# Optimization experiments

Hardware: AMD Instinct MI355X
Metric: run time of the kernel (lower is better)

## Reference

```python
import jax, jax.numpy as jnp
import numpy as np

B, S, D, H = 4, 2048, 1024, 16
DH = D // H


def setup_inputs() -> dict:
    key = jax.random.key(0)
    ks = jax.random.split(key, 11)
    s = 1.0 / np.sqrt(D)
    return {
        "q": jax.random.normal(ks[0], (B, S, D), jnp.float32),
        "k": jax.random.normal(ks[1], (B, S, D), jnp.float32),
        "v": jax.random.normal(ks[2], (B, S, D), jnp.float32),
        "Wq": jax.random.normal(ks[3], (D, D), jnp.float32) * s,
        "bq": jnp.zeros((D,), jnp.float32),
        "Wk": jax.random.normal(ks[4], (D, D), jnp.float32) * s,
        "bk": jnp.zeros((D,), jnp.float32),
        "Wv": jax.random.normal(ks[5], (D, D), jnp.float32) * s,
        "bv": jnp.zeros((D,), jnp.float32),
        "Wo": jax.random.normal(ks[6], (D, D), jnp.float32) * s,
        "bo": jnp.zeros((D,), jnp.float32),
    }


def _split_heads(x):
    # (B, S, D) -> (B, H, S, DH)
    b, s, _ = x.shape
    return x.reshape(b, s, H, DH).transpose(0, 2, 1, 3)


def reference(q, k, v, Wq, bq, Wk, bk, Wv, bv, Wo, bo):
    # torch Linear: x @ W.T + b
    qh = _split_heads(q @ Wq.T + bq)
    kh = _split_heads(k @ Wk.T + bk)
    vh = _split_heads(v @ Wv.T + bv)
    scale = 1.0 / jnp.sqrt(jnp.asarray(DH, qh.dtype))
    scores = jnp.einsum("bhqd,bhkd->bhqk", qh, kh) * scale  # (B,H,S,S)
    probs = jax.nn.softmax(scores, axis=-1)
    ctx = jnp.einsum("bhqk,bhkd->bhqd", probs, vh)  # (B,H,S,DH)
    x = ctx.transpose(0, 2, 1, 3).reshape(q.shape[0], -1, D)
    return x @ Wo.T + bo
```

## Files before the change

kernel.cpp:

```cpp
#include <hip/hip_runtime.h>

typedef __bf16 bf16x8 __attribute__((ext_vector_type(8)));
typedef __bf16 bf16x4 __attribute__((ext_vector_type(4)));
typedef _Float16 f16x4v __attribute__((ext_vector_type(4)));
typedef float f32x4 __attribute__((ext_vector_type(4)));
typedef float f32x16 __attribute__((ext_vector_type(16)));
typedef unsigned short u16;
typedef unsigned int u32;

constexpr int Bc = 4, Sc = 2048, Dc = 1024, Hc = 16, DHc = 64;
constexpr int Mrows = Bc * Sc;
constexpr size_t MK = (size_t)Mrows * Dc;
constexpr size_t WK = (size_t)Dc * Dc;

__device__ __forceinline__ u16 f2bf(float f) {
  u32 u = __float_as_uint(f);
  u = (u + 0x7fffu + ((u >> 16) & 1u)) >> 16;
  return (u16)u;
}

#define LDSP(p) ((__attribute__((address_space(3))) void*)(p))
#define GLBP(p) ((const __attribute__((address_space(1))) void*)(p))

__global__ __launch_bounds__(256) void cvt3_kernel(const float* __restrict__ a,
                                                   const float* __restrict__ b,
                                                   const float* __restrict__ c,
                                                   ushort4* __restrict__ out, int n4) {
  const float4* in = (const float4*)(blockIdx.y == 0 ? a : blockIdx.y == 1 ? b : c);
  ushort4* o = out + (size_t)blockIdx.y * n4;
  int stride = gridDim.x * blockDim.x;
  for (int i = blockIdx.x * blockDim.x + threadIdx.x; i < n4; i += stride) {
    float4 v = in[i];
    ushort4 r;
    r.x = f2bf(v.x); r.y = f2bf(v.y); r.z = f2bf(v.z); r.w = f2bf(v.w);
    o[i] = r;
  }
}

__global__ __launch_bounds__(256) void cvt4_kernel(const float* __restrict__ a,
                                                   const float* __restrict__ b,
                                                   const float* __restrict__ c,
                                                   const float* __restrict__ d,
                                                   ushort4* __restrict__ out, int n4) {
  const float4* in = (const float4*)(blockIdx.y == 0 ? a : blockIdx.y == 1 ? b
                                     : blockIdx.y == 2 ? c : d);
  ushort4* o = out + (size_t)blockIdx.y * n4;
  int stride = gridDim.x * blockDim.x;
  for (int i = blockIdx.x * blockDim.x + threadIdx.x; i < n4; i += stride) {
    float4 v = in[i];
    ushort4 r;
    r.x = f2bf(v.x); r.y = f2bf(v.y); r.z = f2bf(v.z); r.w = f2bf(v.w);
    o[i] = r;
  }
}

enum GemmMode { MODE_Q = 0, MODE_K = 1, MODE_V = 2, MODE_OUT = 3 };

template <int FUSED3>
__global__ __launch_bounds__(512, 2) void gemm8(const u16* __restrict__ A0,
                                                const u16* __restrict__ Bt0,
                                                const float* __restrict__ b0,
                                                const float* __restrict__ b1,
                                                const float* __restrict__ b2,
                                                void* __restrict__ out0) {
  constexpr int K = 1024, NT = 16;
  __shared__ u16 lds[3 * 24576];

  const int y = FUSED3 ? (int)blockIdx.y : 3;
  const u16* A = A0 + (FUSED3 ? (size_t)blockIdx.y * MK : 0);
  const u16* Bt = Bt0 + (FUSED3 ? (size_t)blockIdx.y * WK : 0);
  const float* bias = FUSED3 ? (y == 0 ? b0 : y == 1 ? b1 : b2) : b0;

  const int wg = (blockIdx.x & 7) * 32 + (blockIdx.x >> 3);
  const int tm = wg >> 3, tn = wg & 7;
  const int row0 = tm << 8, col0 = tn << 7;

  const int t_ = threadIdx.x, w = t_ >> 6, l = t_ & 63;
  const int wm = w >> 1, wn = w & 1;
  const int col = l & 31, hh = l >> 5;

  f32x16 acc[2][2] = {};

  auto stA = [&](int tile, int i) {
    u16* buf = &lds[(tile % 3) * 24576];
    const int c = (w * 4 + i) * 64 + l;
    const int r = c >> 3, gl = c & 7;
    __builtin_amdgcn_global_load_lds(
        GLBP(A + (size_t)(row0 + r) * K + (tile << 6) + ((gl ^ (r & 7)) << 3)),
        LDSP(buf + (w * 4 + i) * 512), 16, 0, 0);
  };
  auto stB = [&](int tile, int i) {
    u16* buf = &lds[(tile % 3) * 24576] + 16384;
    const int c = (w * 2 + i) * 64 + l;
    const int r = c >> 3, gl = c & 7;
    __builtin_amdgcn_global_load_lds(
        GLBP(Bt + (size_t)(col0 + r) * K + (tile << 6) + ((gl ^ (r & 7)) << 3)),
        LDSP(buf + (w * 2 + i) * 512), 16, 0, 0);
  };

#pragma unroll
  for (int i = 0; i < 4; ++i) stA(0, i);
#pragma unroll
  for (int i = 0; i < 2; ++i) stB(0, i);
#pragma unroll
  for (int i = 0; i < 4; ++i) stA(1, i);
#pragma unroll
  for (int i = 0; i < 2; ++i) stB(1, i);
  asm volatile("s_waitcnt vmcnt(6)" ::: "memory");
  __builtin_amdgcn_s_barrier();

  const int ar0 = wm * 64 + col, ar1 = ar0 + 32;
  const int br0 = wn * 64 + col, br1 = br0 + 32;

#pragma unroll 1
  for (int t = 0; t < NT; ++t) {
    const u16* abuf = &lds[(t % 3) * 24576];
    const u16* bbuf = abuf + 16384;
#pragma unroll
    for (int ph = 0; ph < 2; ++ph) {
      bf16x8 a0[2], a1[2], q0[2], q1[2];
#pragma unroll
      for (int k2 = 0; k2 < 2; ++k2) {
        const int ks = ph * 2 + k2;
        a0[k2] = *(const bf16x8*)&abuf[ar0 * 64 + ((((ks << 1) + hh) ^ (ar0 & 7)) << 3)];
        a1[k2] = *(const bf16x8*)&abuf[ar1 * 64 + ((((ks << 1) + hh) ^ (ar1 & 7)) << 3)];
        q0[k2] = *(const bf16x8*)&bbuf[br0 * 64 + ((((ks << 1) + hh) ^ (br0 & 7)) << 3)];
        q1[k2] = *(const bf16x8*)&bbuf[br1 * 64 + ((((ks << 1) + hh) ^ (br1 & 7)) << 3)];
      }
      if (t + 2 < NT) {
        if (ph == 0) { stA(t + 2, 0); stA(t + 2, 1); stA(t + 2, 2); }
        else         { stA(t + 2, 3); stB(t + 2, 0); stB(t + 2, 1); }
      }
      __builtin_amdgcn_sched_barrier(0);
      __builtin_amdgcn_s_barrier();
      __builtin_amdgcn_sched_barrier(0);
      __builtin_amdgcn_s_setprio(1);
#pragma unroll
      for (int k2 = 0; k2 < 2; ++k2) {
        acc[0][0] = __builtin_amdgcn_mfma_f32_32x32x16_bf16(a0[k2], q0[k2], acc[0][0], 0, 0, 0);
        acc[0][1] = __builtin_amdgcn_mfma_f32_32x32x16_bf16(a0[k2], q1[k2], acc[0][1], 0, 0, 0);
        acc[1][0] = __builtin_amdgcn_mfma_f32_32x32x16_bf16(a1[k2], q0[k2], acc[1][0], 0, 0, 0);
        acc[1][1] = __builtin_amdgcn_mfma_f32_32x32x16_bf16(a1[k2], q1[k2], acc[1][1], 0, 0, 0);
      }
      __builtin_amdgcn_s_setprio(0);
      __builtin_amdgcn_sched_barrier(0);
    }
    if (t + 2 < NT)      asm volatile("s_waitcnt vmcnt(6)" ::: "memory");
    else if (t + 1 < NT) asm volatile("s_waitcnt vmcnt(0)" ::: "memory");
    __builtin_amdgcn_s_barrier();
  }

#pragma unroll
  for (int mi = 0; mi < 2; ++mi)
#pragma unroll
    for (int ni = 0; ni < 2; ++ni) {
      const int n = col0 + wn * 64 + ni * 32 + col;
      const float bv = bias[n];
      const int mbase = row0 + wm * 64 + mi * 32 + 4 * hh;
      if (y == 3) {
        float* O = (float*)out0;
#pragma unroll
        for (int r = 0; r < 16; ++r) {
          const int m = mbase + (r & 3) + 8 * (r >> 2);
          O[(size_t)m * Dc + n] = acc[mi][ni][r] + bv;
        }
      } else if (y == 2) {
        u16* Vt = (u16*)out0 + 2 * MK;
        const int h = n >> 6, dh = n & 63;
#pragma unroll
        for (int qg = 0; qg < 4; ++qg) {
          const int s0 = mbase + 8 * qg;
          const int b = s0 >> 11, s = s0 & (Sc - 1);
          f16x4v pk;
#pragma unroll
          for (int r4 = 0; r4 < 4; ++r4) pk[r4] = (_Float16)(acc[mi][ni][qg * 4 + r4] + bv);
          *(f16x4v*)&Vt[((size_t)((b * Hc + h) * DHc + dh)) * Sc + s] = pk;
        }
      } else {
        u16* Oh = (u16*)out0 + (size_t)y * MK;
        const float scl = (y == 0) ? 0.125f * 1.44269504089f : 1.f;
        const int h = n >> 6, dh = n & 63;
#pragma unroll
        for (int r = 0; r < 16; ++r) {
          const int m = mbase + (r & 3) + 8 * (r >> 2);
          const int b = m >> 11, s = m & (Sc - 1);
          Oh[((size_t)((b * Hc + h) * Sc + s)) * DHc + dh] = f2bf((acc[mi][ni][r] + bv) * scl);
        }
      }
    }
}

__global__ __launch_bounds__(256, 2) void attn3_kernel(const u16* __restrict__ Qh,
                                                       const u16* __restrict__ Kh,
                                                       const u16* __restrict__ Vt,
                                                       u16* __restrict__ ctx) {
  __shared__ u16 smem[16384];
  u16* K_lds = smem;
  u16* V_lds = smem + 8192;

  const int wid = (blockIdx.x & 7) * 128 + (blockIdx.x >> 3);
  const int qt = wid & 15, bh = wid >> 4;
  const int t = threadIdx.x, w = t >> 6, l = t & 63;
  const int q = l & 31, h = l >> 5;
  const int q0 = qt * 128 + w * 32;

  bf16x8 qf[4];
  {
    const u16* qp = Qh + ((size_t)bh * Sc + q0 + q) * DHc + h * 8;
#pragma unroll
    for (int kk = 0; kk < 4; ++kk) qf[kk] = *(const bf16x8*)(qp + kk * 16);
  }

  f32x16 oacc[2] = {};
  float m_run = -3.0e38f, l_run = 0.f;

  for (int kt = 0; kt < Sc; kt += 128) {
    __syncthreads();
#pragma unroll
    for (int c = 0; c < 4; ++c) {
      const int kb = (w * 4 + c) * 8;
      const int row = kb + (l >> 3);
      const int sg = (l & 7) ^ (row & 7);
      __builtin_amdgcn_global_load_lds(GLBP(Kh + ((size_t)bh * Sc + kt + row) * DHc + sg * 8),
                                       LDSP(&K_lds[kb * 64]), 16, 0, 0);
    }
#pragma unroll
    for (int c = 0; c < 4; ++c) {
      const int vb = (w * 4 + c) * 4;
      const int row = vb + (l >> 4);
      const int sg = (l & 15) ^ (row & 15);
      __builtin_amdgcn_global_load_lds(GLBP(Vt + ((size_t)bh * DHc + row) * Sc + kt + sg * 8),
                                       LDSP(&V_lds[vb * 128]), 16, 0, 0);
    }
    __syncthreads();

#pragma unroll
    for (int h64 = 0; h64 < 2; ++h64) {
      f32x16 sacc[2];
#pragma unroll
      for (int kt32 = 0; kt32 < 2; ++kt32) {
        f32x16 s_ = {};
        const int krow = h64 * 64 + kt32 * 32 + q;
        __builtin_amdgcn_s_setprio(1);
#pragma unroll
        for (int kk = 0; kk < 4; ++kk) {
          bf16x8 kf = *(const bf16x8*)&K_lds[krow * 64 + ((2 * kk + h) ^ (krow & 7)) * 8];
          s_ = __builtin_amdgcn_mfma_f32_32x32x16_bf16(kf, qf[kk], s_, 0, 0, 0);
        }
        __builtin_amdgcn_s_setprio(0);
        sacc[kt32] = s_;
      }

      float mx = sacc[0][0];
#pragma unroll
      for (int r = 1; r < 16; ++r) mx = fmaxf(mx, sacc[0][r]);
#pragma unroll
      for (int r = 0; r < 16; ++r) mx = fmaxf(mx, sacc[1][r]);
      mx = fmaxf(mx, __shfl_xor(mx, 32));
      if (__any(mx - m_run > 8.f)) {
        const float mnew = fmaxf(m_run, mx);
        const float corr = __builtin_amdgcn_exp2f(m_run - mnew);
        m_run = mnew;
        l_run *= corr;
#pragma unroll
        for (int dt = 0; dt < 2; ++dt)
#pragma unroll
          for (int r = 0; r < 16; ++r) oacc[dt][r] *= corr;
      }
      float sum = 0.f;
      f16x4v pa[2][4];
#pragma unroll
      for (int kt32 = 0; kt32 < 2; ++kt32)
#pragma unroll
        for (int kc = 0; kc < 4; ++kc)
#pragma unroll
          for (int j = 0; j < 4; ++j) {
            float pv = __builtin_amdgcn_exp2f(sacc[kt32][kc * 4 + j] - m_run);
            sum += pv;
            pa[kt32][kc][j] = (_Float16)pv;
          }
      sum += __shfl_xor(sum, 32);
      l_run += sum;

      __builtin_amdgcn_s_setprio(1);
#pragma unroll
      for (int kt32 = 0; kt32 < 2; ++kt32)
#pragma unroll
        for (int kc = 0; kc < 4; ++kc)
#pragma unroll
          for (int dt = 0; dt < 2; ++dt) {
            const int vrow = dt * 32 + q;
            const int kslot = h64 * 8 + kt32 * 4 + kc;
            f16x4v vf = *(const f16x4v*)&V_lds[vrow * 128 + ((kslot ^ (vrow & 15)) * 8) + 4 * h];
            oacc[dt] = __builtin_amdgcn_mfma_f32_32x32x8f16(vf, pa[kt32][kc], oacc[dt], 0, 0, 0);
          }
      __builtin_amdgcn_s_setprio(0);
    }
  }

  __syncthreads();
  const float inv = 1.f / l_run;
  u16* E = smem + w * 2048;
#pragma unroll
  for (int dt = 0; dt < 2; ++dt)
#pragma unroll
    for (int rg = 0; rg < 4; ++rg) {
      bf16x4 pk;
#pragma unroll
      for (int j = 0; j < 4; ++j) pk[j] = (__bf16)(oacc[dt][rg * 4 + j] * inv);
      const int dh0 = dt * 32 + rg * 8 + 4 * h;
      int byte = q * 128 + dh0 * 2;
      byte ^= (q & 7) << 4;
      *(bf16x4*)((char*)E + byte) = pk;
    }
  __syncthreads();
  const int b = bh >> 4, head = bh & 15;
  const size_t crow = ((size_t)(b * Sc + q0 + q)) * Dc + head * 64 + h * 32;
#pragma unroll
  for (int i = 0; i < 4; ++i) {
    const int g = (4 * h + i) ^ (q & 7);
    uint4 tv = *(const uint4*)((char*)E + q * 128 + g * 16);
    *(uint4*)((u16*)ctx + crow + i * 8) = tv;
  }
}

extern "C" void kernel_launch(void* const* d_in, const int* in_sizes, int n_in,
                              void* d_out, int out_size, void* d_ws, size_t ws_size,
                              hipStream_t stream) {
  const float* q  = (const float*)d_in[0];
  const float* k  = (const float*)d_in[1];
  const float* v  = (const float*)d_in[2];
  const float* Wq = (const float*)d_in[3];
  const float* bq = (const float*)d_in[4];
  const float* Wk = (const float*)d_in[5];
  const float* bk = (const float*)d_in[6];
  const float* Wv = (const float*)d_in[7];
  const float* bv = (const float*)d_in[8];
  const float* Wo = (const float*)d_in[9];
  const float* bo = (const float*)d_in[10];
  float* out = (float*)d_out;

  u16* qb  = (u16*)d_ws;
  u16* Wqb = qb + 3 * MK;
  u16* Qh  = Wqb + 4 * WK;
  u16* Kh  = Qh + MK;
  u16* VtB = Kh + MK;
  u16* ctx = VtB + MK;

  cvt3_kernel<<<dim3(2048, 3), 256, 0, stream>>>(q, k, v, (ushort4*)qb, (int)(MK / 4));
  cvt4_kernel<<<dim3(512, 4), 256, 0, stream>>>(Wq, Wk, Wv, Wo, (ushort4*)Wqb, (int)(WK / 4));

  gemm8<1><<<dim3(256, 3), 512, 0, stream>>>(qb, Wqb, bq, bk, bv, (void*)Qh);

  attn3_kernel<<<1024, 256, 0, stream>>>(Qh, Kh, VtB, ctx);

  gemm8<0><<<dim3(256, 1), 512, 0, stream>>>(ctx, Wqb + 3 * WK, bo, bo, bo, (void*)out);
}
```

Before: 236.6 us.

## Double-buffer attention K/V tiles and use permlane-swapped 32x32x16 f16 MFMA for PV

Measured after the change: 220.5 us. 1.07x faster.

```diff
diff --git a/kernel.cpp b/kernel.cpp
--- a/kernel.cpp
+++ b/kernel.cpp
@@ -2,11 +2,13 @@
 
 typedef __bf16 bf16x8 __attribute__((ext_vector_type(8)));
 typedef __bf16 bf16x4 __attribute__((ext_vector_type(4)));
+typedef _Float16 f16x8 __attribute__((ext_vector_type(8)));
 typedef _Float16 f16x4v __attribute__((ext_vector_type(4)));
 typedef float f32x4 __attribute__((ext_vector_type(4)));
 typedef float f32x16 __attribute__((ext_vector_type(16)));
 typedef unsigned short u16;
 typedef unsigned int u32;
+typedef unsigned int u32x4 __attribute__((ext_vector_type(4)));
 
 constexpr int Bc = 4, Sc = 2048, Dc = 1024, Hc = 16, DHc = 64;
 constexpr int Mrows = Bc * Sc;
@@ -53,8 +55,6 @@
     o[i] = r;
   }
 }
-
-enum GemmMode { MODE_Q = 0, MODE_K = 1, MODE_V = 2, MODE_OUT = 3 };
 
 template <int FUSED3>
 __global__ __launch_bounds__(512, 2) void gemm8(const u16* __restrict__ A0,
@@ -190,7 +190,7 @@
     }
 }
 
-__global__ __launch_bounds__(256, 2) void attn3_kernel(const u16* __restrict__ Qh,
+__global__ __launch_bounds__(256, 4) void attn4_kernel(const u16* __restrict__ Qh,
                                                        const u16* __restrict__ Kh,
                                                        const u16* __restrict__ Vt,
                                                        u16* __restrict__ ctx) {
@@ -214,91 +214,101 @@
   f32x16 oacc[2] = {};
   float m_run = -3.0e38f, l_run = 0.f;
 
-  for (int kt = 0; kt < Sc; kt += 128) {
-    __syncthreads();
-#pragma unroll
-    for (int c = 0; c < 4; ++c) {
-      const int kb = (w * 4 + c) * 8;
-      const int row = kb + (l >> 3);
-      const int sg = (l & 7) ^ (row & 7);
+  const int lrow = l >> 3, lg = l & 7;
+
+  auto stage = [&](int tile, int buf) {
+    const int kt = tile << 6;
+    u16* Kb = K_lds + buf * 4096;
+    u16* Vb = V_lds + buf * 4096;
+#pragma unroll
+    for (int c = 0; c < 2; ++c) {
+      const int rb = w * 16 + c * 8;
+      const int row = rb + lrow;
+      const int sg = lg ^ (row & 7);
       __builtin_amdgcn_global_load_lds(GLBP(Kh + ((size_t)bh * Sc + kt + row) * DHc + sg * 8),
-                                       LDSP(&K_lds[kb * 64]), 16, 0, 0);
-    }
-#pragma unroll
-    for (int c = 0; c < 4; ++c) {
-      const int vb = (w * 4 + c) * 4;
-      const int row = vb + (l >> 4);
-      const int sg = (l & 15) ^ (row & 15);
+                                       LDSP(&Kb[rb * 64]), 16, 0, 0);
       __builtin_amdgcn_global_load_lds(GLBP(Vt + ((size_t)bh * DHc + row) * Sc + kt + sg * 8),
-                                       LDSP(&V_lds[vb * 128]), 16, 0, 0);
-    }
-    __syncthreads();
-
-#pragma unroll
-    for (int h64 = 0; h64 < 2; ++h64) {
-      f32x16 sacc[2];
-#pragma unroll
-      for (int kt32 = 0; kt32 < 2; ++kt32) {
-        f32x16 s_ = {};
-        const int krow = h64 * 64 + kt32 * 32 + q;
+                                       LDSP(&Vb[rb * 64]), 16, 0, 0);
+    }
+  };
+
+  stage(0, 0);
+  __syncthreads();
+
+#pragma unroll 1
+  for (int tile = 0; tile < 32; ++tile) {
+    const int cur = tile & 1;
+    if (tile + 1 < 32) stage(tile + 1, cur ^ 1);
+    const u16* Kb = K_lds + cur * 4096;
+    const u16* Vb = V_lds + cur * 4096;
+
+    f32x16 sacc[2] = {};
+    __builtin_amdgcn_s_setprio(1);
+#pragma unroll
+    for (int kk = 0; kk < 4; ++kk) {
+      const int kr0 = q, kr1 = 32 + q;
+      bf16x8 kf0 = *(const bf16x8*)&Kb[kr0 * 64 + ((2 * kk + h) ^ (kr0 & 7)) * 8];
+      bf16x8 kf1 = *(const bf16x8*)&Kb[kr1 * 64 + ((2 * kk + h) ^ (kr1 & 7)) * 8];
+      sacc[0] = __builtin_amdgcn_mfma_f32_32x32x16_bf16(kf0, qf[kk], sacc[0], 0, 0, 0);
+      sacc[1] = __builtin_amdgcn_mfma_f32_32x32x16_bf16(kf1, qf[kk], sacc[1], 0, 0, 0);
+    }
+    __builtin_amdgcn_s_setprio(0);
+
+    float mx = sacc[0][0];
+#pragma unroll
+    for (int r = 1; r < 16; ++r) mx = fmaxf(mx, sacc[0][r]);
+#pragma unroll
+    for (int r = 0; r < 16; ++r) mx = fmaxf(mx, sacc[1][r]);
+    mx = fmaxf(mx, __shfl_xor(mx, 32));
+    if (__any(mx - m_run > 8.f)) {
+      const float mnew = fmaxf(m_run, mx);
+      const float corr = __builtin_amdgcn_exp2f(m_run - mnew);
+      m_run = mnew;
+      l_run *= corr;
+#pragma unroll
+      for (int dt = 0; dt < 2; ++dt)
+#pragma unroll
+        for (int r = 0; r < 16; ++r) oacc[dt][r] *= corr;
+    }
+
+    float sum = 0.f;
+#pragma unroll
+    for (int kt32 = 0; kt32 < 2; ++kt32)
+#pragma unroll
+      for (int c = 0; c < 2; ++c) {
+        float p0 = __builtin_amdgcn_exp2f(sacc[kt32][c * 8 + 0] - m_run);
+        float p1 = __builtin_amdgcn_exp2f(sacc[kt32][c * 8 + 1] - m_run);
+        float p2 = __builtin_amdgcn_exp2f(sacc[kt32][c * 8 + 2] - m_run);
+        float p3 = __builtin_amdgcn_exp2f(sacc[kt32][c * 8 + 3] - m_run);
+        float p4 = __builtin_amdgcn_exp2f(sacc[kt32][c * 8 + 4] - m_run);
+        float p5 = __builtin_amdgcn_exp2f(sacc[kt32][c * 8 + 5] - m_run);
+        float p6 = __builtin_amdgcn_exp2f(sacc[kt32][c * 8 + 6] - m_run);
+        float p7 = __builtin_amdgcn_exp2f(sacc[kt32][c * 8 + 7] - m_run);
+        sum += ((p0 + p1) + (p2 + p3)) + ((p4 + p5) + (p6 + p7));
+        u32 X0 = __builtin_bit_cast(u32, __builtin_amdgcn_cvt_pkrtz(p0, p1));
+        u32 X1 = __builtin_bit_cast(u32, __builtin_amdgcn_cvt_pkrtz(p2, p3));
+        u32 Y0 = __builtin_bit_cast(u32, __builtin_amdgcn_cvt_pkrtz(p4, p5));
+        u32 Y1 = __builtin_bit_cast(u32, __builtin_amdgcn_cvt_pkrtz(p6, p7));
+        auto rA = __builtin_amdgcn_permlane32_swap(X0, Y0, false, false);
+        auto rB = __builtin_amdgcn_permlane32_swap(X1, Y1, false, false);
+        u32x4 wv;
+        wv[0] = rA[0]; wv[1] = rB[0]; wv[2] = rA[1]; wv[3] = rB[1];
+        f16x8 pf = __builtin_bit_cast(f16x8, wv);
+        const int gb = kt32 * 4 + c * 2 + h;
         __builtin_amdgcn_s_setprio(1);
 #pragma unroll
-        for (int kk = 0; kk < 4; ++kk) {
-          bf16x8 kf = *(const bf16x8*)&K_lds[krow * 64 + ((2 * kk + h) ^ (krow & 7)) * 8];
-          s_ = __builtin_amdgcn_mfma_f32_32x32x16_bf16(kf, qf[kk], s_, 0, 0, 0);
+        for (int dt = 0; dt < 2; ++dt) {
+          const int vrow = dt * 32 + q;
+          f16x8 vf = *(const f16x8*)&Vb[vrow * 64 + ((gb ^ (vrow & 7)) * 8)];
+          oacc[dt] = __builtin_amdgcn_mfma_f32_32x32x16_f16(vf, pf, oacc[dt], 0, 0, 0);
         }
         __builtin_amdgcn_s_setprio(0);
-        sacc[kt32] = s_;
-      }
-
-      float mx = sacc[0][0];
-#pragma unroll
-      for (int r = 1; r < 16; ++r) mx = fmaxf(mx, sacc[0][r]);
-#pragma unroll
-      for (int r = 0; r < 16; ++r) mx = fmaxf(mx, sacc[1][r]);
-      mx = fmaxf(mx, __shfl_xor(mx, 32));
-      if (__any(mx - m_run > 8.f)) {
-        const float mnew = fmaxf(m_run, mx);
-        const float corr = __builtin_amdgcn_exp2f(m_run - mnew);
-        m_run = mnew;
-        l_run *= corr;
-#pragma unroll
-        for (int dt = 0; dt < 2; ++dt)
-#pragma unroll
-          for (int r = 0; r < 16; ++r) oacc[dt][r] *= corr;
-      }
-      float sum = 0.f;
-      f16x4v pa[2][4];
-#pragma unroll
-      for (int kt32 = 0; kt32 < 2; ++kt32)
-#pragma unroll
-        for (int kc = 0; kc < 4; ++kc)
-#pragma unroll
-          for (int j = 0; j < 4; ++j) {
-            float pv = __builtin_amdgcn_exp2f(sacc[kt32][kc * 4 + j] - m_run);
-            sum += pv;
-            pa[kt32][kc][j] = (_Float16)pv;
-          }
-      sum += __shfl_xor(sum, 32);
-      l_run += sum;
-
-      __builtin_amdgcn_s_setprio(1);
-#pragma unroll
-      for (int kt32 = 0; kt32 < 2; ++kt32)
-#pragma unroll
-        for (int kc = 0; kc < 4; ++kc)
-#pragma unroll
-          for (int dt = 0; dt < 2; ++dt) {
-            const int vrow = dt * 32 + q;
-            const int kslot = h64 * 8 + kt32 * 4 + kc;
-            f16x4v vf = *(const f16x4v*)&V_lds[vrow * 128 + ((kslot ^ (vrow & 15)) * 8) + 4 * h];
-            oacc[dt] = __builtin_amdgcn_mfma_f32_32x32x8f16(vf, pa[kt32][kc], oacc[dt], 0, 0, 0);
-          }
-      __builtin_amdgcn_s_setprio(0);
-    }
-  }
-
-  __syncthreads();
+      }
+    sum += __shfl_xor(sum, 32);
+    l_run += sum;
+    __syncthreads();
+  }
+
   const float inv = 1.f / l_run;
   u16* E = smem + w * 2048;
 #pragma unroll
@@ -352,7 +362,7 @@
 
   gemm8<1><<<dim3(256, 3), 512, 0, stream>>>(qb, Wqb, bq, bk, bv, (void*)Qh);
 
-  attn3_kernel<<<1024, 256, 0, stream>>>(Qh, Kh, VtB, ctx);
+  attn4_kernel<<<1024, 256, 0, stream>>>(Qh, Kh, VtB, ctx);
 
   gemm8<0><<<dim3(256, 1), 512, 0, stream>>>(ctx, Wqb + 3 * WK, bo, bo, bo, (void*)out);
 }
```
